# Performance work log

Hardware: AMD Instinct MI355X
Metric: run time of the kernel (lower is better)

The kernel has to match this reference:

```python
import jax, jax.numpy as jnp
import numpy as np


def setup_inputs() -> dict:
    key = jax.random.key(0)
    k1, k2 = jax.random.split(key)
    B, N, D, OUT = 4, 8192, 64, 64
    inputs = jax.random.normal(k1, (B, N, D), dtype=jnp.float32)
    kernel = jax.random.normal(k2, (D, OUT), dtype=jnp.float32) * (1.0 / np.sqrt(D))
    return {"inputs": inputs, "kernel": kernel}


def reference(inputs, kernel):
    # sim = X X^T  -> [B, N, N] dense similarity (unscaled self-attention, V = X)
    sim = jnp.einsum("bnd,bmd->bnm", inputs, inputs)
    A = jax.nn.softmax(sim, axis=-1)          # row-wise softmax over neighbors
    h = jnp.einsum("bnm,bmd->bnd", A, inputs)  # aggregate
    return jnp.einsum("bnd,do->bno", h, kernel)  # output projection
```

## Files before the change

### kernel.cpp

```cpp
#include <hip/hip_runtime.h>
#include <math.h>

typedef _Float16 f16;
typedef _Float16 f16x2 __attribute__((ext_vector_type(2)));
typedef _Float16 f16x4 __attribute__((ext_vector_type(4)));
typedef _Float16 f16x8 __attribute__((ext_vector_type(8)));
typedef float    f32x4  __attribute__((ext_vector_type(4)));
typedef float    f32x16 __attribute__((ext_vector_type(16)));

#define PKRTZ(a, b) __builtin_bit_cast(f16x2, __builtin_amdgcn_cvt_pkrtz((a), (b)))
#define MFMA32(a, b, c) __builtin_amdgcn_mfma_f32_32x32x16_f16((a), (b), (c), 0, 0, 0)

#define NN 8192
#define DD 64
#define KT 32
#define NQB 64
#define NWAVES 4
#define KPW (NN / NWAVES)
#define NTILES (KPW / KT)

#define LOG2E 1.44269504088896f

__device__ __forceinline__ int sig32(int k) {
  const int g = (k >> 2) & 3;
  return (g == 1 || g == 2) ? (k ^ 12) : k;
}

__global__ __launch_bounds__(256, 2)
void prep_f16(const float* __restrict__ X, f16* __restrict__ Xk, f16* __restrict__ Xv)
{
  __shared__ f16 Lt[64 * 72];
  const int tid  = threadIdx.x;
  const int b    = blockIdx.x >> 7;
  const int kb64 = (blockIdx.x & 127) * 64;

  {
    const int r = tid >> 2;
    const int c = (tid & 3) * 16;
    const float* p = X + ((size_t)(b * NN + kb64 + r)) * DD + c;
    const float4 a0 = *(const float4*)(p);
    const float4 a1 = *(const float4*)(p + 4);
    const float4 a2 = *(const float4*)(p + 8);
    const float4 a3 = *(const float4*)(p + 12);
    f16x8 v0, v1;
    v0[0]=(f16)a0.x; v0[1]=(f16)a0.y; v0[2]=(f16)a0.z; v0[3]=(f16)a0.w;
    v0[4]=(f16)a1.x; v0[5]=(f16)a1.y; v0[6]=(f16)a1.z; v0[7]=(f16)a1.w;
    v1[0]=(f16)a2.x; v1[1]=(f16)a2.y; v1[2]=(f16)a2.z; v1[3]=(f16)a2.w;
    v1[4]=(f16)a3.x; v1[5]=(f16)a3.y; v1[6]=(f16)a3.z; v1[7]=(f16)a3.w;
    *(f16x8*)&Lt[r * 72 + c]     = v0;
    *(f16x8*)&Lt[r * 72 + c + 8] = v1;
  }
  __syncthreads();

  #pragma unroll
  for (int i = 0; i < 2; ++i) {
    const int gc  = i * 256 + tid;
    const int h   = gc >> 8;
    const int ci  = gc & 255;
    const int c   = ci >> 6;
    const int ln  = ci & 63;
    const int hi  = ln >> 5;
    const int l31 = ln & 31;
    const int row = h * 32 + sig32(l31);
    const f16x8 v = *(const f16x8*)&Lt[row * 72 + c * 16 + hi * 8];
    const int kt  = (kb64 >> 5) + h;
    *(f16x8*)(Xk + ((size_t)(b * (NN/32) + kt)) * 2048 + ci * 8) = v;
  }

  #pragma unroll
  for (int i = 0; i < 2; ++i) {
    const int gc  = i * 256 + tid;
    const int h   = gc >> 8;
    const int ci  = gc & 255;
    const int ins = ci >> 6;
    const int db  = ins >> 1;
    const int kh  = ins & 1;
    const int ln  = ci & 63;
    const int hi  = ln >> 5;
    const int l31 = ln & 31;
    union { f16 s[8]; f16x8 v; } u;
    #pragma unroll
    for (int j = 0; j < 8; ++j)
      u.s[j] = Lt[(h*32 + kh*16 + hi*8 + j) * 72 + db*32 + l31];
    const int kt = (kb64 >> 5) + h;
    *(f16x8*)(Xv + ((size_t)(b * (NN/32) + kt)) * 2048 + ci * 8) = u.v;
  }
}

#define HL_PITCH 68
#define WL_OFF  (64 * HL_PITCH * 4)
#define LST_OFF (2 * 64 * HL_PITCH * 4)
#define SMEM_B  (LST_OFF + 64 * 4)

__global__ __launch_bounds__(256, 2)
void gconv_attn(const float* __restrict__ X, const f16* __restrict__ Xk,
                const f16* __restrict__ Xv, const float* __restrict__ W,
                float* __restrict__ out)
{
  __shared__ __align__(16) unsigned char smem[SMEM_B];

  const int tid  = threadIdx.x;
  const int lane = tid & 63;
  const int wave = tid >> 6;
  const int l31  = lane & 31;
  const int hi   = lane >> 5;

  const int xcd   = blockIdx.x & 7;
  const int slot  = blockIdx.x >> 3;
  const int batch = xcd >> 1;
  const int qblk  = slot * 2 + (xcd & 1);
  const int qbase = qblk * NQB;
  const float* Xb = X + (size_t)batch * NN * DD;

  const f16* XkW = Xk + ((size_t)batch * (NN/32) + wave * NTILES) * 2048 + lane * 8;
  const f16* XvW = Xv + ((size_t)batch * (NN/32) + wave * NTILES) * 2048 + lane * 8;

  f16x8 qf[2][4];
  f32x16 minit[2];
  float lrow[2];
  #pragma unroll
  for (int qb = 0; qb < 2; ++qb) {
    const float* qp = Xb + (size_t)(qbase + qb*32 + l31) * DD + hi*8;
    float nrm = 0.f;
    #pragma unroll
    for (int c = 0; c < 4; ++c) {
      const float4 a = *(const float4*)(qp + c*16);
      const float4 b = *(const float4*)(qp + c*16 + 4);
      float xs[8] = {a.x, a.y, a.z, a.w, b.x, b.y, b.z, b.w};
      f16x8 v;
      #pragma unroll
      for (int e = 0; e < 8; ++e) {
        const f16 kv = (f16)xs[e];
        const f16 qs = (f16)(xs[e] * LOG2E);
        nrm += (float)qs * (float)kv;
        v[e] = qs;
      }
      qf[qb][c] = v;
    }
    nrm += __shfl_xor(nrm, 32);
    const float m2 = nrm + 2.0f;
    #pragma unroll
    for (int e = 0; e < 16; ++e) minit[qb][e] = -m2;
    lrow[qb] = 0.f;
  }

  f32x16 acc[2][2];
  #pragma unroll
  for (int a = 0; a < 2; ++a)
    #pragma unroll
    for (int b = 0; b < 2; ++b)
      #pragma unroll
      for (int e = 0; e < 16; ++e) acc[a][b][e] = 0.f;

  const f16x2 kOnes = (f16x2){(f16)1.0f, (f16)1.0f};

  f16x8 kaA[4], kaB[4];
  f16x8 vbA[2][2], vbB[2][2];

  auto LDK = [&](f16x8 (&ka)[4], int t) {
    const f16* kn = XkW + (size_t)t * 2048;
    #pragma unroll
    for (int c = 0; c < 4; ++c)
      ka[c] = *(const f16x8*)(kn + c * 512);
  };
  auto LDV = [&](f16x8 (&vb)[2][2], int t) {
    const f16* vn = XvW + (size_t)t * 2048;
    #pragma unroll
    for (int db = 0; db < 2; ++db)
      #pragma unroll
      for (int kh = 0; kh < 2; ++kh)
        vb[db][kh] = *(const f16x8*)(vn + (db*2 + kh) * 512);
  };

  auto SMpack = [&](const f32x16& s, float& lr, f16x8& paLo, f16x8& paHi) {
    float p[16];
    #pragma unroll
    for (int r = 0; r < 16; ++r) p[r] = __builtin_amdgcn_exp2f(s[r]);
    union { f16x8 v; f16x2 h[4]; } a, b;
    a.h[0] = PKRTZ(p[0],  p[1]);  a.h[1] = PKRTZ(p[2],  p[3]);
    a.h[2] = PKRTZ(p[4],  p[5]);  a.h[3] = PKRTZ(p[6],  p[7]);
    b.h[0] = PKRTZ(p[8],  p[9]);  b.h[1] = PKRTZ(p[10], p[11]);
    b.h[2] = PKRTZ(p[12], p[13]); b.h[3] = PKRTZ(p[14], p[15]);
    float la = 0.f, lb = 0.f;
    #pragma unroll
    for (int i = 0; i < 4; ++i) {
      la = __builtin_amdgcn_fdot2(a.h[i], kOnes, la, false);
      lb = __builtin_amdgcn_fdot2(b.h[i], kOnes, lb, false);
    }
    lr += la + lb;
    paLo = a.v; paHi = b.v;
  };

  auto TILE = [&](f16x8 (&ka)[4], f16x8 (&vb)[2][2], int tpf) {
    f32x16 s0 = MFMA32(ka[0], qf[0][0], minit[0]);
    s0 = MFMA32(ka[1], qf[0][1], s0);
    s0 = MFMA32(ka[2], qf[0][2], s0);
    s0 = MFMA32(ka[3], qf[0][3], s0);
    f32x16 s1 = MFMA32(ka[0], qf[1][0], minit[1]);
    s1 = MFMA32(ka[1], qf[1][1], s1);
    s1 = MFMA32(ka[2], qf[1][2], s1);
    s1 = MFMA32(ka[3], qf[1][3], s1);

    LDK(ka, tpf);

    f16x8 pa00, pa01, pa10, pa11;
    SMpack(s0, lrow[0], pa00, pa01);
    SMpack(s1, lrow[1], pa10, pa11);

    acc[0][0] = MFMA32(pa00, vb[0][0], acc[0][0]);
    acc[0][0] = MFMA32(pa01, vb[0][1], acc[0][0]);
    acc[0][1] = MFMA32(pa00, vb[1][0], acc[0][1]);
    acc[0][1] = MFMA32(pa01, vb[1][1], acc[0][1]);
    acc[1][0] = MFMA32(pa10, vb[0][0], acc[1][0]);
    acc[1][0] = MFMA32(pa11, vb[0][1], acc[1][0]);
    acc[1][1] = MFMA32(pa10, vb[1][0], acc[1][1]);
    acc[1][1] = MFMA32(pa11, vb[1][1], acc[1][1]);

    LDV(vb, tpf);
  };

  LDK(kaA, 0); LDV(vbA, 0);
  LDK(kaB, 1); LDV(vbB, 1);

  for (int t = 0; t < NTILES; t += 2) {
    const int ta = (t + 2 < NTILES) ? t + 2 : NTILES - 1;
    const int tb = (t + 3 < NTILES) ? t + 3 : NTILES - 1;
    TILE(kaA, vbA, ta);
    TILE(kaB, vbB, tb);
  }

  __syncthreads();
  float* Hl    = (float*)smem;
  float* Wl    = (float*)(smem + WL_OFF);
  float* Lstar = (float*)(smem + LST_OFF);

  for (int i = tid; i < 64*HL_PITCH; i += 256) Hl[i] = 0.f;
  for (int i = tid; i < 64*64; i += 256) Wl[(i >> 6)*HL_PITCH + (i & 63)] = W[i];
  if (tid < 64) Lstar[tid] = 0.f;
  __syncthreads();

  #pragma unroll
  for (int qb = 0; qb < 2; ++qb) {
    float lr = lrow[qb];
    lr += __shfl_xor(lr, 32);
    if (lane < 32) atomicAdd(&Lstar[qb*32 + lane], lr);
    #pragma unroll
    for (int db = 0; db < 2; ++db)
      #pragma unroll
      for (int r = 0; r < 16; ++r) {
        const int ql = (r & 3) + 8*(r >> 2) + 4*hi;
        atomicAdd(&Hl[(db*32 + l31)*HL_PITCH + qb*32 + ql], acc[qb][db][r]);
      }
  }
  __syncthreads();

  {
    const int qq = tid >> 2;
    const int og = (tid & 3) * 16;
    f32x4 o[4];
    #pragma unroll
    for (int i = 0; i < 4; ++i) o[i] = (f32x4){0.f,0.f,0.f,0.f};
    for (int d = 0; d < 64; ++d) {
      const float h = Hl[d*HL_PITCH + qq];
      const f32x4* wr = (const f32x4*)&Wl[d*HL_PITCH + og];
      #pragma unroll
      for (int i = 0; i < 4; ++i) o[i] += h * wr[i];
    }
    const float inv = 1.0f / Lstar[qq];
    float* op = out + ((size_t)batch * NN + qbase + qq) * DD + og;
    #pragma unroll
    for (int i = 0; i < 4; ++i)
      *(f32x4*)(op + i*4) = o[i] * inv;
  }
}

extern "C" void kernel_launch(void* const* d_in, const int* in_sizes, int n_in,
                              void* d_out, int out_size, void* d_ws, size_t ws_size,
                              hipStream_t stream) {
  const float* X = (const float*)d_in[0];
  const float* W = (const float*)d_in[1];
  float* out = (float*)d_out;

  f16* Xk = (f16*)d_ws;
  f16* Xv = (f16*)((char*)d_ws + (size_t)4 * NN * DD * 2);
  prep_f16<<<dim3(512), dim3(256), 0, stream>>>(X, Xk, Xv);
  gconv_attn<<<dim3(512), dim3(256), 0, stream>>>(X, Xk, Xv, W, out);
}
```

Before: 176.2 us.

## Software-pipeline QK MFMA one tile ahead of softmax and PV

Restructures the main loop so the QK^T MFMAs for the next key tile are issued before the softmax and PV MFMAs of the current tile. This lets matrix-core work overlap the exp and pack VALU work and hides MFMA latency. The max-subtraction moves from the MFMA accumulator init into the exp argument, and K fragments are now single-buffered while more score registers stay live. That adds a VALU subtract per element and raises register pressure, which could cut occupancy.

```diff
diff --git a/kernel.cpp b/kernel.cpp
--- a/kernel.cpp
+++ b/kernel.cpp
@@ -116,7 +116,7 @@
   const f16* XvW = Xv + ((size_t)batch * (NN/32) + wave * NTILES) * 2048 + lane * 8;
 
   f16x8 qf[2][4];
-  f32x16 minit[2];
+  float m2[2];
   float lrow[2];
   #pragma unroll
   for (int qb = 0; qb < 2; ++qb) {
@@ -138,9 +138,7 @@
       qf[qb][c] = v;
     }
     nrm += __shfl_xor(nrm, 32);
-    const float m2 = nrm + 2.0f;
-    #pragma unroll
-    for (int e = 0; e < 16; ++e) minit[qb][e] = -m2;
+    m2[qb] = nrm + 2.0f;
     lrow[qb] = 0.f;
   }
 
@@ -152,12 +150,16 @@
       #pragma unroll
       for (int e = 0; e < 16; ++e) acc[a][b][e] = 0.f;
 
+  f32x16 z16;
+  #pragma unroll
+  for (int e = 0; e < 16; ++e) z16[e] = 0.f;
+
   const f16x2 kOnes = (f16x2){(f16)1.0f, (f16)1.0f};
 
-  f16x8 kaA[4], kaB[4];
+  f16x8 ka[4];
   f16x8 vbA[2][2], vbB[2][2];
 
-  auto LDK = [&](f16x8 (&ka)[4], int t) {
+  auto LDK = [&](int t) {
     const f16* kn = XkW + (size_t)t * 2048;
     #pragma unroll
     for (int c = 0; c < 4; ++c)
@@ -172,10 +174,21 @@
         vb[db][kh] = *(const f16x8*)(vn + (db*2 + kh) * 512);
   };
 
-  auto SMpack = [&](const f32x16& s, float& lr, f16x8& paLo, f16x8& paHi) {
+  auto QK = [&](f32x16& s0, f32x16& s1) {
+    s0 = MFMA32(ka[0], qf[0][0], z16);
+    s0 = MFMA32(ka[1], qf[0][1], s0);
+    s0 = MFMA32(ka[2], qf[0][2], s0);
+    s0 = MFMA32(ka[3], qf[0][3], s0);
+    s1 = MFMA32(ka[0], qf[1][0], z16);
+    s1 = MFMA32(ka[1], qf[1][1], s1);
+    s1 = MFMA32(ka[2], qf[1][2], s1);
+    s1 = MFMA32(ka[3], qf[1][3], s1);
+  };
+
+  auto SMpack = [&](const f32x16& s, float m2v, float& lr, f16x8& paLo, f16x8& paHi) {
     float p[16];
     #pragma unroll
-    for (int r = 0; r < 16; ++r) p[r] = __builtin_amdgcn_exp2f(s[r]);
+    for (int r = 0; r < 16; ++r) p[r] = __builtin_amdgcn_exp2f(s[r] - m2v);
     union { f16x8 v; f16x2 h[4]; } a, b;
     a.h[0] = PKRTZ(p[0],  p[1]);  a.h[1] = PKRTZ(p[2],  p[3]);
     a.h[2] = PKRTZ(p[4],  p[5]);  a.h[3] = PKRTZ(p[6],  p[7]);
@@ -191,43 +204,40 @@
     paLo = a.v; paHi = b.v;
   };
 
-  auto TILE = [&](f16x8 (&ka)[4], f16x8 (&vb)[2][2], int tpf) {
-    f32x16 s0 = MFMA32(ka[0], qf[0][0], minit[0]);
-    s0 = MFMA32(ka[1], qf[0][1], s0);
-    s0 = MFMA32(ka[2], qf[0][2], s0);
-    s0 = MFMA32(ka[3], qf[0][3], s0);
-    f32x16 s1 = MFMA32(ka[0], qf[1][0], minit[1]);
-    s1 = MFMA32(ka[1], qf[1][1], s1);
-    s1 = MFMA32(ka[2], qf[1][2], s1);
-    s1 = MFMA32(ka[3], qf[1][3], s1);
-
-    LDK(ka, tpf);
-
-    f16x8 pa00, pa01, pa10, pa11;
-    SMpack(s0, lrow[0], pa00, pa01);
-    SMpack(s1, lrow[1], pa10, pa11);
-
-    acc[0][0] = MFMA32(pa00, vb[0][0], acc[0][0]);
-    acc[0][0] = MFMA32(pa01, vb[0][1], acc[0][0]);
-    acc[0][1] = MFMA32(pa00, vb[1][0], acc[0][1]);
-    acc[0][1] = MFMA32(pa01, vb[1][1], acc[0][1]);
-    acc[1][0] = MFMA32(pa10, vb[0][0], acc[1][0]);
-    acc[1][0] = MFMA32(pa11, vb[0][1], acc[1][0]);
-    acc[1][1] = MFMA32(pa10, vb[1][0], acc[1][1]);
-    acc[1][1] = MFMA32(pa11, vb[1][1], acc[1][1]);
-
-    LDV(vb, tpf);
-  };
-
-  LDK(kaA, 0); LDV(vbA, 0);
-  LDK(kaB, 1); LDV(vbB, 1);
-
-  for (int t = 0; t < NTILES; t += 2) {
-    const int ta = (t + 2 < NTILES) ? t + 2 : NTILES - 1;
-    const int tb = (t + 3 < NTILES) ? t + 3 : NTILES - 1;
-    TILE(kaA, vbA, ta);
-    TILE(kaB, vbB, tb);
-  }
+  auto SMPV = [&](const f32x16& s0, const f32x16& s1, const f16x8 (&vb)[2][2]) {
+    f16x8 pa0, pa1;
+    SMpack(s0, m2[0], lrow[0], pa0, pa1);
+    acc[0][0] = MFMA32(pa0, vb[0][0], acc[0][0]);
+    acc[0][0] = MFMA32(pa1, vb[0][1], acc[0][0]);
+    acc[0][1] = MFMA32(pa0, vb[1][0], acc[0][1]);
+    acc[0][1] = MFMA32(pa1, vb[1][1], acc[0][1]);
+    f16x8 pb0, pb1;
+    SMpack(s1, m2[1], lrow[1], pb0, pb1);
+    acc[1][0] = MFMA32(pb0, vb[0][0], acc[1][0]);
+    acc[1][0] = MFMA32(pb1, vb[0][1], acc[1][0]);
+    acc[1][1] = MFMA32(pb0, vb[1][0], acc[1][1]);
+    acc[1][1] = MFMA32(pb1, vb[1][1], acc[1][1]);
+  };
+
+  f32x16 sE0, sE1, sO0, sO1;
+  LDK(0);
+  LDV(vbA, 0);
+  LDV(vbB, 1);
+  QK(sE0, sE1);
+  LDK(1);
+  for (int t = 1; t < NTILES - 1; t += 2) {
+    QK(sO0, sO1);
+    LDK(t + 1);
+    SMPV(sE0, sE1, vbA);
+    LDV(vbA, t + 1);
+    QK(sE0, sE1);
+    LDK(t + 2);
+    SMPV(sO0, sO1, vbB);
+    LDV(vbB, t + 2);
+  }
+  QK(sO0, sO1);
+  SMPV(sE0, sE1, vbA);
+  SMPV(sO0, sO1, vbB);
 
   __syncthreads();
   float* Hl    = (float*)smem;
```

Result: faster. 164.7 us (-6.5%).
